# Kernel optimization log

Measured on AMD Instinct MI355X. Metric: run time of the kernel, lower is better.

## Reference

```python
import jax, jax.numpy as jnp
import numpy as np

B, L, D, H = 2, 2048, 512, 8
SAMPLING_FACTOR = 5


def setup_inputs() -> dict:
    key = jax.random.key(0)
    ks = jax.random.split(key, 12)
    L_K = min(8000, L)
    log_L_K = int(np.ceil(np.log1p(L_K)))
    U_part = min(SAMPLING_FACTOR * L * log_L_K, L_K)  # = 2048
    inp = {
        'q': jax.random.normal(ks[0], (B, L, D), jnp.float32),
        'k': jax.random.normal(ks[1], (B, L, D), jnp.float32),
        'v': jax.random.normal(ks[2], (B, L, D), jnp.float32),
        'Wq': jax.random.normal(ks[3], (D, D), jnp.float32) * 0.02,
        'bq': jnp.zeros((D,), jnp.float32),
        'Wk': jax.random.normal(ks[4], (D, D), jnp.float32) * 0.02,
        'bk': jnp.zeros((D,), jnp.float32),
        'Wv': jax.random.normal(ks[5], (D, D), jnp.float32) * 0.02,
        'bv': jnp.zeros((D,), jnp.float32),
        'Wo': jax.random.normal(ks[6], (D, D), jnp.float32) * 0.02,
        'bo': jnp.zeros((D,), jnp.float32),
        'index_sample': jax.random.randint(ks[7], (U_part,), 0, L_K, jnp.int32),
    }
    return inp


def _prob_sparse(qh, Kh, Vh, index_sample):
    # qh, Kh, Vh: [B, H, L, d]
    L_K = min(8000, Kh.shape[2])  # K_sample = K[:, :8000]; L_K = its length
    L_Q = qh.shape[2]
    Ks = Kh[:, :, index_sample, :]                                  # [B,H,U,d]
    QKs = jnp.einsum('bhqd,bhkd->bhqk', qh, Ks)                     # [B,H,Lq,U]
    # M = max - sum/L_K  (source divides by L_K, not U_part)
    M = QKs.max(axis=-1) - QKs.sum(axis=-1) / L_K                   # [B,H,Lq]
    u = min(SAMPLING_FACTOR * int(np.ceil(np.log1p(L_Q))), L_Q)     # = 40
    _, M_top = jax.lax.top_k(-M, u)                                 # topk(largest=False)
    Q_red = jnp.take_along_axis(qh, M_top[..., None], axis=2)       # [B,H,u,d]
    d_k = qh.shape[-1]
    scores = jnp.einsum('bhqd,bhkd->bhqk', Q_red, Kh) / jnp.sqrt(jnp.asarray(d_k, qh.dtype))
    probs = jax.nn.softmax(scores, axis=-1)
    out = jnp.einsum('bhqk,bhkd->bhqd', probs, Vh)                  # [B,H,u,d]
    return out, scores


def reference(q, k, v, Wq, bq, Wk, bk, Wv, bv, Wo, bo, index_sample):
    qp = q @ Wq.T + bq
    kp = k @ Wk.T + bk
    vp = v @ Wv.T + bv
    Bsz, Lq, Dm = qp.shape
    d = Dm // H
    # faithful to source: q is view'd to [B,H,Lq,d] WITHOUT transpose
    qh = qp.reshape(Bsz, H, Lq, d)
    kh = kp.reshape(Bsz, -1, H, d).transpose(0, 2, 1, 3)
    vh = vp.reshape(Bsz, -1, H, d).transpose(0, 2, 1, 3)
    out, _ = _prob_sparse(qh, kh, vh, index_sample)
    u = out.shape[2]
    out = out.transpose(0, 2, 1, 3).reshape(Bsz, u, Dm)             # concat
    return out @ Wo.T + bo                                          # [B,u,D]
```

## Files before the change

### kernel.cpp

```cpp
#include <hip/hip_runtime.h>
#include <math.h>

#define B_ 2
#define L_ 2048
#define D_ 512
#define H_ 8
#define DH 64
#define NS 2048
#define NU 40
#define BHD (L_*D_)
#define QHS (L_*DH)
#define WSPM 786432

typedef __attribute__((ext_vector_type(8))) short bf16x8;
typedef __attribute__((ext_vector_type(4))) float f32x4;

__device__ inline float4 ld4(const float* p) { return *reinterpret_cast<const float4*>(p); }

__device__ inline unsigned short hi16(float x) { return (unsigned short)(__float_as_uint(x) >> 16); }
__device__ inline float trunchf(float x) { return __uint_as_float(__float_as_uint(x) & 0xFFFF0000u); }
__device__ inline void tsplit(float x, unsigned short& hs, unsigned short& ms, unsigned short& ls) {
  float h = trunchf(x); hs = hi16(x);
  float r = x - h;
  float m = trunchf(r); ms = hi16(r);
  float r2 = r - m;
  ls = hi16(r2);
}

__global__ __launch_bounds__(256) void wsplit(const float* __restrict__ Wq,
                                              const float* __restrict__ Wk,
                                              const float* __restrict__ Wv,
                                              unsigned short* __restrict__ dst,
                                              int matArg) {
  const int mat = (matArg >= 0) ? matArg : (int)blockIdx.y;
  const float* W = (mat == 0) ? Wq : (mat == 1) ? Wk : Wv;
  unsigned short* d = dst + ((matArg >= 0) ? 0 : (size_t)mat * WSPM);
  const int t = threadIdx.x;
  const int nt = blockIdx.x >> 3, g16 = blockIdx.x & 7;
  const int kc = t >> 4, lr = t & 15;
  const int n = nt*128 + g16*16 + lr;
  const float* src = W + (size_t)n*512 + kc*32;
  float xs[32];
#pragma unroll
  for (int i = 0; i < 8; ++i) {
    float4 v4 = ld4(src + 4*i);
    xs[4*i] = v4.x; xs[4*i+1] = v4.y; xs[4*i+2] = v4.z; xs[4*i+3] = v4.w;
  }
  unsigned short Hs[32], Ms[32], Ls[32];
#pragma unroll
  for (int e = 0; e < 32; ++e) tsplit(xs[e], Hs[e], Ms[e], Ls[e]);
#pragma unroll
  for (int p = 0; p < 3; ++p) {
    const unsigned short* sp = (p == 0) ? Hs : (p == 1) ? Ms : Ls;
    unsigned short* base = d + ((size_t)((p*4 + nt)*8 + g16)*16 + kc)*512;
#pragma unroll
    for (int lg = 0; lg < 4; ++lg) {
      union { bf16x8 v; unsigned short u[8]; } P;
#pragma unroll
      for (int e = 0; e < 8; ++e) P.u[e] = sp[lg*8 + e];
      *reinterpret_cast<bf16x8*>(base + (lr + 16*lg)*8) = P.v;
    }
  }
}

__global__ __launch_bounds__(256) void proj_mfma2(
    const float* __restrict__ qa, const float* __restrict__ ka, const float* __restrict__ va,
    const unsigned short* __restrict__ wsp,
    const float* __restrict__ bq, const float* __restrict__ bk, const float* __restrict__ bv,
    float* __restrict__ qp, float* __restrict__ kp, float* __restrict__ vp,
    int matArg)
{
  __shared__ __align__(16) unsigned short a3[3][128][36];
  const int t = threadIdx.x;
  const int mat = (matArg >= 0) ? matArg : (int)blockIdx.z;
  const float* A    = (mat == 0) ? qa : (mat == 1) ? ka : va;
  const float* bias = (mat == 0) ? bq : (mat == 1) ? bk : bv;
  float* C          = (mat == 0) ? qp : (mat == 1) ? kp : vp;
  const unsigned short* wspm = wsp + ((matArg >= 0) ? 0 : (size_t)mat * WSPM);
  const int m0 = blockIdx.x * 128, nt = blockIdx.y;
  const int w = t >> 6, l = t & 63;
  const int wm = w >> 1, wn = w & 1;
  const int lr = l & 15, lg = l >> 4;
  const int srow = t >> 1, sc0 = (t & 1) * 16;

  f32x4 acc[4][4];
#pragma unroll
  for (int i = 0; i < 4; ++i)
#pragma unroll
    for (int j = 0; j < 4; ++j) acc[i][j] = (f32x4){0.f, 0.f, 0.f, 0.f};

  for (int kc = 0; kc < 16; ++kc) {
    __syncthreads();
    bf16x8 bw[3][4];
#pragma unroll
    for (int p = 0; p < 3; ++p)
#pragma unroll
      for (int ni = 0; ni < 4; ++ni)
        bw[p][ni] = *reinterpret_cast<const bf16x8*>(
            wspm + ((size_t)((p*4 + nt)*8 + wn*4 + ni)*16 + kc)*512 + l*8);
    {
      const float* src = A + (size_t)(m0 + srow) * 512 + kc*32 + sc0;
      float xs[16];
#pragma unroll
      for (int i = 0; i < 4; ++i) {
        float4 v4 = ld4(src + 4*i);
        xs[4*i] = v4.x; xs[4*i+1] = v4.y; xs[4*i+2] = v4.z; xs[4*i+3] = v4.w;
      }
#pragma unroll
      for (int hh = 0; hh < 2; ++hh) {
        union { bf16x8 v; unsigned short u[8]; } H, M, L;
#pragma unroll
        for (int e = 0; e < 8; ++e) tsplit(xs[hh*8 + e], H.u[e], M.u[e], L.u[e]);
        *reinterpret_cast<bf16x8*>(&a3[0][srow][sc0 + 8*hh]) = H.v;
        *reinterpret_cast<bf16x8*>(&a3[1][srow][sc0 + 8*hh]) = M.v;
        *reinterpret_cast<bf16x8*>(&a3[2][srow][sc0 + 8*hh]) = L.v;
      }
    }
    __syncthreads();

#pragma unroll
    for (int mi = 0; mi < 4; ++mi) {
      bf16x8 a0 = *reinterpret_cast<const bf16x8*>(&a3[0][wm*64 + mi*16 + lr][lg*8]);
      bf16x8 a1 = *reinterpret_cast<const bf16x8*>(&a3[1][wm*64 + mi*16 + lr][lg*8]);
      bf16x8 a2 = *reinterpret_cast<const bf16x8*>(&a3[2][wm*64 + mi*16 + lr][lg*8]);
#pragma unroll
      for (int ni = 0; ni < 4; ++ni) {
        acc[mi][ni] = __builtin_amdgcn_mfma_f32_16x16x32_bf16(a0, bw[0][ni], acc[mi][ni], 0, 0, 0);
        acc[mi][ni] = __builtin_amdgcn_mfma_f32_16x16x32_bf16(a0, bw[1][ni], acc[mi][ni], 0, 0, 0);
        acc[mi][ni] = __builtin_amdgcn_mfma_f32_16x16x32_bf16(a1, bw[0][ni], acc[mi][ni], 0, 0, 0);
        acc[mi][ni] = __builtin_amdgcn_mfma_f32_16x16x32_bf16(a1, bw[1][ni], acc[mi][ni], 0, 0, 0);
        acc[mi][ni] = __builtin_amdgcn_mfma_f32_16x16x32_bf16(a0, bw[2][ni], acc[mi][ni], 0, 0, 0);
        acc[mi][ni] = __builtin_amdgcn_mfma_f32_16x16x32_bf16(a2, bw[0][ni], acc[mi][ni], 0, 0, 0);
      }
    }
  }
#pragma unroll
  for (int mi = 0; mi < 4; ++mi)
#pragma unroll
    for (int ni = 0; ni < 4; ++ni) {
      const int gn = nt*128 + wn*64 + ni*16 + lr;
      const float bv_ = bias[gn];
#pragma unroll
      for (int r = 0; r < 4; ++r) {
        const int gm = m0 + wm*64 + mi*16 + lg*4 + r;
        C[(size_t)gm * 512 + gn] = acc[mi][ni][r] + bv_;
      }
    }
}

__global__ __launch_bounds__(1024) void ksum_kernel(const float* __restrict__ kp,
                                                    const int* __restrict__ idx,
                                                    float* __restrict__ ksum) {
  __shared__ float part[16][64];
  const int bh = blockIdx.x;
  const int b = bh >> 3, h = bh & 7;
  const int t = threadIdx.x;
  const int sg = t >> 6, j = t & 63;
  const float* kbase = kp + (size_t)b*BHD + h*DH;
  float a = 0.f;
  for (int s = sg*128; s < sg*128 + 128; ++s)
    a += kbase[(size_t)idx[s]*512 + j];
  part[sg][j] = a;
  __syncthreads();
  if (t < 64) {
    float s = 0.f;
#pragma unroll
    for (int i = 0; i < 16; ++i) s += part[i][t];
    ksum[bh*64 + t] = s;
  }
}

__global__ __launch_bounds__(256, 2) void m_kernel(const float* __restrict__ qp,
                                                   const float* __restrict__ kp,
                                                   const int* __restrict__ idx,
                                                   float* __restrict__ Mp) {
  __shared__ __align__(16) unsigned short k3[3][128][72];
  const int t = threadIdx.x;
  const int bid = blockIdx.x;
  const int bh = bid >> 5, qt = (bid >> 2) & 7, ks = bid & 3;
  const int b = bh >> 3, h = bh & 7;
  const int w = t >> 6, l = t & 63;
  const int lr = l & 15;
  const int lg = l >> 4;

  bf16x8 qf[4][2][3];
  {
    const float* qbase = qp + (size_t)b*BHD + (size_t)h*QHS + (size_t)(qt*256 + w*64 + lr) * 64 + lg*8;
#pragma unroll
    for (int mi = 0; mi < 4; ++mi)
#pragma unroll
      for (int c = 0; c < 2; ++c) {
        const float* src = qbase + mi*16*64 + c*32;
        float4 x0 = ld4(src), x1 = ld4(src + 4);
        float xs[8] = {x0.x, x0.y, x0.z, x0.w, x1.x, x1.y, x1.z, x1.w};
        union { bf16x8 v; unsigned short u[8]; } H, M, L;
#pragma unroll
        for (int e = 0; e < 8; ++e) tsplit(xs[e], H.u[e], M.u[e], L.u[e]);
        qf[mi][c][0] = H.v; qf[mi][c][1] = M.v; qf[mi][c][2] = L.v;
      }
  }

  const float* kbase = kp + (size_t)b*BHD + h*DH;
  const int ib = ks * 512;
  const int srow = t >> 1, sh = (t & 1) * 32;

  float4 vst[8];
  {
    const int kr = idx[ib + srow];
    const float* src = kbase + (size_t)kr * 512 + sh;
#pragma unroll
    for (int i = 0; i < 8; ++i) vst[i] = ld4(src + 4*i);
  }

  float mx[4][4];
#pragma unroll
  for (int mi = 0; mi < 4; ++mi)
#pragma unroll
    for (int r = 0; r < 4; ++r) mx[mi][r] = -INFINITY;

  for (int tl = 0; tl < 4; ++tl) {
    __syncthreads();
    {
#pragma unroll
      for (int e2 = 0; e2 < 4; ++e2) {
        union { bf16x8 v; unsigned short u[8]; } H, M, L;
        float xs[8] = {vst[2*e2].x, vst[2*e2].y, vst[2*e2].z, vst[2*e2].w,
                       vst[2*e2+1].x, vst[2*e2+1].y, vst[2*e2+1].z, vst[2*e2+1].w};
#pragma unroll
        for (int e = 0; e < 8; ++e) tsplit(xs[e], H.u[e], M.u[e], L.u[e]);
        *reinterpret_cast<bf16x8*>(&k3[0][srow][sh + 8*e2]) = H.v;
        *reinterpret_cast<bf16x8*>(&k3[1][srow][sh + 8*e2]) = M.v;
        *reinterpret_cast<bf16x8*>(&k3[2][srow][sh + 8*e2]) = L.v;
      }
    }
    if (tl < 3) {
      const int kr = idx[ib + (tl+1)*128 + srow];
      const float* src = kbase + (size_t)kr * 512 + sh;
#pragma unroll
      for (int i = 0; i < 8; ++i) vst[i] = ld4(src + 4*i);
    }
    __syncthreads();

    for (int n2 = 0; n2 < 4; ++n2) {
      bf16x8 bf[2][3][2];
#pragma unroll
      for (int ns = 0; ns < 2; ++ns)
#pragma unroll
        for (int p = 0; p < 3; ++p)
#pragma unroll
          for (int c = 0; c < 2; ++c)
            bf[ns][p][c] = *reinterpret_cast<const bf16x8*>(&k3[p][n2*32 + ns*16 + lr][c*32 + lg*8]);
      __builtin_amdgcn_s_setprio(1);
#pragma unroll
      for (int mi = 0; mi < 4; ++mi)
#pragma unroll
        for (int ns = 0; ns < 2; ++ns) {
          f32x4 acc = {0.f, 0.f, 0.f, 0.f};
#pragma unroll
          for (int c = 0; c < 2; ++c) acc = __builtin_amdgcn_mfma_f32_16x16x32_bf16(qf[mi][c][0], bf[ns][0][c], acc, 0, 0, 0);
#pragma unroll
          for (int c = 0; c < 2; ++c) acc = __builtin_amdgcn_mfma_f32_16x16x32_bf16(qf[mi][c][0], bf[ns][1][c], acc, 0, 0, 0);
#pragma unroll
          for (int c = 0; c < 2; ++c) acc = __builtin_amdgcn_mfma_f32_16x16x32_bf16(qf[mi][c][1], bf[ns][0][c], acc, 0, 0, 0);
#pragma unroll
          for (int c = 0; c < 2; ++c) acc = __builtin_amdgcn_mfma_f32_16x16x32_bf16(qf[mi][c][1], bf[ns][1][c], acc, 0, 0, 0);
#pragma unroll
          for (int c = 0; c < 2; ++c) acc = __builtin_amdgcn_mfma_f32_16x16x32_bf16(qf[mi][c][0], bf[ns][2][c], acc, 0, 0, 0);
#pragma unroll
          for (int c = 0; c < 2; ++c) acc = __builtin_amdgcn_mfma_f32_16x16x32_bf16(qf[mi][c][2], bf[ns][0][c], acc, 0, 0, 0);
#pragma unroll
          for (int r = 0; r < 4; ++r) mx[mi][r] = fmaxf(mx[mi][r], acc[r]);
        }
      __builtin_amdgcn_s_setprio(0);
    }
  }

#pragma unroll
  for (int mi = 0; mi < 4; ++mi)
#pragma unroll
    for (int r = 0; r < 4; ++r) {
      float v = mx[mi][r];
      v = fmaxf(v, __shfl_xor(v, 1));
      v = fmaxf(v, __shfl_xor(v, 2));
      v = fmaxf(v, __shfl_xor(v, 4));
      v = fmaxf(v, __shfl_xor(v, 8));
      if (lr == 0)
        Mp[ks*32768 + bh*2048 + qt*256 + w*64 + mi*16 + lg*4 + r] = v;
    }
}

__global__ __launch_bounds__(256) void topk_kernel(const float* __restrict__ qp,
                                                   const float* __restrict__ ksum,
                                                   const float* __restrict__ Mp,
                                                   int* __restrict__ Mtop) {
  __shared__ float ks_s[64];
  __shared__ unsigned hist[256];
  __shared__ int wsum[4];
  __shared__ unsigned bitmap[64];
  __shared__ unsigned long long comb[NU];
  __shared__ int s_sel, s_rem, s_cnt;
  const int bh = blockIdx.x;
  const int b = bh >> 3, h = bh & 7;
  const int t = threadIdx.x;
  if (t < 64) ks_s[t] = ksum[bh*64 + t];
  __syncthreads();

  unsigned mykey[8];
#pragma unroll
  for (int c = 0; c < 8; ++c) {
    const int qi = c * 256 + t;
    const float* qrow = qp + (size_t)b*BHD + (size_t)h*QHS + (size_t)qi * 64;
    float dot = 0.f;
#pragma unroll
    for (int cc = 0; cc < 16; ++cc) {
      float4 q4 = ld4(qrow + 4 * cc);
      dot += q4.x * ks_s[4*cc + 0];
      dot += q4.y * ks_s[4*cc + 1];
      dot += q4.z * ks_s[4*cc + 2];
      dot += q4.w * ks_s[4*cc + 3];
    }
    const float mx2 = fmaxf(fmaxf(Mp[bh*2048 + qi], Mp[32768 + bh*2048 + qi]),
                            fmaxf(Mp[65536 + bh*2048 + qi], Mp[98304 + bh*2048 + qi]));
    const float m = mx2 - dot * (1.0f/2048.0f);
    const unsigned u = __float_as_uint(m);
    mykey[c] = (u >> 31) ? ~u : (u | 0x80000000u);
  }

  unsigned prefMask = 0u, prefVal = 0u;
  int rem = NU;
  for (int shift = 24; shift >= 0; shift -= 8) {
    hist[t] = 0;
    __syncthreads();
#pragma unroll
    for (int c = 0; c < 8; ++c) {
      const unsigned key = mykey[c];
      if ((key & prefMask) == prefVal)
        atomicAdd(&hist[(key >> shift) & 255], 1u);
    }
    __syncthreads();
    const int binc = (int)hist[t];
    int inc = binc;
#pragma unroll
    for (int off = 1; off < 64; off <<= 1) {
      const int nb = __shfl_up(inc, off);
      if ((t & 63) >= off) inc += nb;
    }
    if ((t & 63) == 63) wsum[t >> 6] = inc;
    __syncthreads();
    int wadd = 0;
    for (int w2 = 0; w2 < (t >> 6); ++w2) wadd += wsum[w2];
    const int incl = inc + wadd;
    const int excl = incl - binc;
    if (excl < rem && rem <= incl) { s_sel = t; s_rem = rem - excl; }
    __syncthreads();
    prefVal |= ((unsigned)s_sel) << shift;
    prefMask |= 0xFFu << shift;
    rem = s_rem;
    __syncthreads();
  }
  const unsigned T = prefVal;

  if (t < 64) bitmap[t] = 0;
  if (t == 0) s_cnt = 0;
  __syncthreads();
#pragma unroll
  for (int c = 0; c < 8; ++c) {
    const unsigned key = mykey[c];
    const int qi = c * 256 + t;
    if (key < T) {
      const int pos = atomicAdd(&s_cnt, 1);
      comb[pos] = ((unsigned long long)key << 11) | (unsigned)qi;
    } else if (key == T) {
      atomicOr(&bitmap[qi >> 5], 1u << (qi & 31));
    }
  }
  __syncthreads();
  if (t == 0) {
    int need = rem, cpos = s_cnt;
    for (int wd = 0; wd < 64 && need > 0; ++wd) {
      unsigned bits = bitmap[wd];
      while (bits && need > 0) {
        const int bit = __ffs(bits) - 1;
        bits &= bits - 1;
        comb[cpos++] = ((unsigned long long)T << 11) | (unsigned)(wd*32 + bit);
        --need;
      }
    }
  }
  __syncthreads();

  if (t < 64) {
    const unsigned long long mine = (t < NU) ? comb[t] : ~0ULL;
    int rank = 0;
#pragma unroll
    for (int step = 1; step < 64; ++step) {
      const unsigned long long other = __shfl(mine, (t + step) & 63);
      rank += (other < mine) ? 1 : 0;
    }
    if (t < NU) Mtop[bh*NU + rank] = (int)(mine & 0x7FFu);
  }
}

__global__ __launch_bounds__(256) void flash_partial(const float* __restrict__ qp,
                                                     const float* __restrict__ kp,
                                                     const float* __restrict__ vp,
                                                     const int* __restrict__ Mtop,
                                                     float* __restrict__ pm,
                                                     float* __restrict__ pl,
                                                     float* __restrict__ pacc) {
  __shared__ float qr[NU][65];
  __shared__ float kv[64][65];
  __shared__ float sl[NU][65];
  __shared__ float ms[NU], ls[NU], fs[NU];
  const int bid = blockIdx.x;
  const int bh = bid >> 4, kt = bid & 15;
  const int b = bh >> 3, h = bh & 7;
  const int t = threadIdx.x;
  const int g = t >> 6, j = t & 63;
  const int r4 = t >> 2, sub = t & 3;

  {
    const float* qbase = qp + (size_t)b*BHD + (size_t)h*QHS;
#pragma unroll
    for (int r = 0; r < 10; ++r) {
      const int q = g*10 + r;
      qr[q][j] = qbase[(size_t)Mtop[bh*NU + q]*64 + j];
    }
  }
  if (t < NU) { ms[t] = -INFINITY; ls[t] = 0.f; }
  float acc[10];
#pragma unroll
  for (int r = 0; r < 10; ++r) acc[r] = 0.f;

  const float* kbase = kp + (size_t)b*BHD + h*DH;
  const float* vbase = vp + (size_t)b*BHD + h*DH;
  const int srow = t >> 2, scb = (t & 3)*16;

  for (int st = 0; st < 2; ++st) {
    const int kb = kt*128 + st*64;
    __syncthreads();
    {
      const float* src = kbase + (size_t)(kb + srow)*512 + scb;
#pragma unroll
      for (int i = 0; i < 4; ++i) {
        float4 v = ld4(src + 4*i);
        kv[srow][scb + 4*i + 0] = v.x;
        kv[srow][scb + 4*i + 1] = v.y;
        kv[srow][scb + 4*i + 2] = v.z;
        kv[srow][scb + 4*i + 3] = v.w;
      }
    }
    __syncthreads();
    {
      float sv[10];
#pragma unroll
      for (int r = 0; r < 10; ++r) {
        const int q = g*10 + r;
        float s = 0.f;
#pragma unroll 8
        for (int jj = 0; jj < 64; ++jj) s += qr[q][jj]*kv[j][jj];
        sv[r] = s * 0.125f;
      }
#pragma unroll
      for (int r = 0; r < 10; ++r) sl[g*10 + r][j] = sv[r];
    }
    __syncthreads();
    float4 vst[4];
    {
      const float* src = vbase + (size_t)(kb + srow)*512 + scb;
#pragma unroll
      for (int i = 0; i < 4; ++i) vst[i] = ld4(src + 4*i);
    }
    if (r4 < NU) {
      float tm = -INFINITY;
#pragma unroll
      for (int c = 0; c < 16; ++c) tm = fmaxf(tm, sl[r4][sub*16 + c]);
      tm = fmaxf(tm, __shfl_xor(tm, 1));
      tm = fmaxf(tm, __shfl_xor(tm, 2));
      const float nm = fmaxf(ms[r4], tm);
      if (sub == 0) { fs[r4] = expf(ms[r4] - nm); ms[r4] = nm; }
    }
    __syncthreads();
    {
#pragma unroll
      for (int r = 0; r < 10; ++r) {
        const int q = g*10 + r;
        acc[r] *= fs[q];
        sl[q][j] = expf(sl[q][j] - ms[q]);
      }
#pragma unroll
      for (int i = 0; i < 4; ++i) {
        kv[srow][scb + 4*i + 0] = vst[i].x;
        kv[srow][scb + 4*i + 1] = vst[i].y;
        kv[srow][scb + 4*i + 2] = vst[i].z;
        kv[srow][scb + 4*i + 3] = vst[i].w;
      }
    }
    __syncthreads();
    if (r4 < NU) {
      float s = 0.f;
#pragma unroll
      for (int c = 0; c < 16; ++c) s += sl[r4][sub*16 + c];
      s += __shfl_xor(s, 1);
      s += __shfl_xor(s, 2);
      if (sub == 0) ls[r4] = ls[r4]*fs[r4] + s;
    }
    {
#pragma unroll 4
      for (int kk = 0; kk < 64; ++kk) {
        const float vv = kv[kk][j];
#pragma unroll
        for (int r = 0; r < 10; ++r) acc[r] += sl[g*10 + r][kk]*vv;
      }
    }
  }
  __syncthreads();
  const size_t base = (size_t)(bh*16 + kt)*NU;
  if (t < NU) { pm[base + t] = ms[t]; pl[base + t] = ls[t]; }
#pragma unroll
  for (int r = 0; r < 10; ++r)
    pacc[(base + g*10 + r)*64 + j] = acc[r];
}

__global__ __launch_bounds__(256) void flash_combine(const float* __restrict__ pm,
                                                     const float* __restrict__ pl,
                                                     const float* __restrict__ pacc,
                                                     float* __restrict__ outc) {
  const int t = threadIdx.x;
  const int qg = t >> 6, j = t & 63;
  const int bh = blockIdx.x / 10;
  const int q  = (blockIdx.x % 10)*4 + qg;
  const int b = bh >> 3, h = bh & 7;
  float m = -INFINITY;
#pragma unroll
  for (int kt = 0; kt < 16; ++kt) m = fmaxf(m, pm[(size_t)(bh*16 + kt)*NU + q]);
  float Lsum = 0.f, num = 0.f;
#pragma unroll
  for (int kt = 0; kt < 16; ++kt) {
    const size_t base = (size_t)(bh*16 + kt)*NU;
    const float w = expf(pm[base + q] - m);
    Lsum += w * pl[base + q];
    num  += w * pacc[(base + q)*64 + j];
  }
  outc[(size_t)(b*NU + q)*512 + h*64 + j] = num / Lsum;
}

__global__ __launch_bounds__(256) void wo_gemm(const float* __restrict__ outc,
                                               const float* __restrict__ Wo,
                                               float* __restrict__ pwo) {
  __shared__ __align__(16) float a_t[80][68];
  __shared__ __align__(16) float w_t[64][68];
  const int t = threadIdx.x;
  const int ty = t >> 4, tx = t & 15;
  const int nt = blockIdx.x, ks = blockIdx.y;
  float acc[5][4];
#pragma unroll
  for (int i = 0; i < 5; ++i)
#pragma unroll
    for (int j = 0; j < 4; ++j) acc[i][j] = 0.f;

  for (int c = 0; c < 2; ++c) {
    const int kb = ks*128 + c*64;
    __syncthreads();
#pragma unroll
    for (int i = 0; i < 20; ++i) {
      const int fi = t + 256*i;
      const int row = fi >> 6, col = fi & 63;
      a_t[row][col] = outc[(size_t)row*512 + kb + col];
    }
#pragma unroll
    for (int i = 0; i < 16; ++i) {
      const int fi = t + 256*i;
      const int row = fi >> 6, col = fi & 63;
      w_t[row][col] = Wo[(size_t)(nt*64 + row)*512 + kb + col];
    }
    __syncthreads();
    for (int gq = 0; gq < 16; ++gq) {
      float4 av[5], wv[4];
#pragma unroll
      for (int i = 0; i < 5; ++i) av[i] = *reinterpret_cast<const float4*>(&a_t[ty + 16*i][4*gq]);
#pragma unroll
      for (int j = 0; j < 4; ++j) wv[j] = *reinterpret_cast<const float4*>(&w_t[tx + 16*j][4*gq]);
#pragma unroll
      for (int i = 0; i < 5; ++i)
#pragma unroll
        for (int j = 0; j < 4; ++j) {
          acc[i][j] += av[i].x * wv[j].x;
          acc[i][j] += av[i].y * wv[j].y;
          acc[i][j] += av[i].z * wv[j].z;
          acc[i][j] += av[i].w * wv[j].w;
        }
    }
  }
#pragma unroll
  for (int i = 0; i < 5; ++i)
#pragma unroll
    for (int j = 0; j < 4; ++j)
      pwo[ks*40960 + (size_t)(ty + 16*i)*512 + nt*64 + tx + 16*j] = acc[i][j];
}

__global__ __launch_bounds__(256) void wo_combine(const float* __restrict__ pwo,
                                                  const float* __restrict__ bo,
                                                  float* __restrict__ out) {
  const int gi = blockIdx.x*256 + threadIdx.x;
  const float4* p = reinterpret_cast<const float4*>(pwo);
  const float4 a = p[gi], b4 = p[10240 + gi], c4 = p[20480 + gi], d4 = p[30720 + gi];
  const float4 bb = ld4(bo + 4*(gi & 127));
  float4 o;
  o.x = a.x + b4.x + c4.x + d4.x + bb.x;
  o.y = a.y + b4.y + c4.y + d4.y + bb.y;
  o.z = a.z + b4.z + c4.z + d4.z + bb.z;
  o.w = a.w + b4.w + c4.w + d4.w + bb.w;
  reinterpret_cast<float4*>(out)[gi] = o;
}

extern "C" void kernel_launch(void* const* d_in, const int* in_sizes, int n_in,
                              void* d_out, int out_size, void* d_ws, size_t ws_size,
                              hipStream_t stream) {
  const float* q  = (const float*)d_in[0];
  const float* k  = (const float*)d_in[1];
  const float* v  = (const float*)d_in[2];
  const float* Wq = (const float*)d_in[3];
  const float* bq = (const float*)d_in[4];
  const float* Wk = (const float*)d_in[5];
  const float* bk = (const float*)d_in[6];
  const float* Wv = (const float*)d_in[7];
  const float* bv = (const float*)d_in[8];
  const float* Wo = (const float*)d_in[9];
  const float* bo = (const float*)d_in[10];
  const int*  idx = (const int*)d_in[11];

  float* ws   = (float*)d_ws;
  float* qp   = ws;
  float* kp   = ws + 2097152;
  float* vp   = ws + 4194304;
  float* ksum = ws + 6291456;
  int*   Mtop = (int*)(ws + 6292480);
  float* pm   = ws + 6293120;
  float* pl   = ws + 6303360;
  float* pacc = ws + 6313600;
  float* outc = ws + 6968960;
  float* Mp   = pm;
  float* pwo  = pm;
  unsigned short* wsp = (unsigned short*)(ws + 6291456);

  const dim3 blk(256);
  const bool bigws = (ws_size >= (size_t)7471104 * 4);
  if (bigws) {
    wsplit<<<dim3(32, 3), blk, 0, stream>>>(Wq, Wk, Wv, wsp, -1);
    proj_mfma2<<<dim3(32, 4, 3), blk, 0, stream>>>(q, k, v, wsp, bq, bk, bv, qp, kp, vp, -1);
  } else {
    for (int m = 0; m < 3; ++m) {
      wsplit<<<dim3(32, 1), blk, 0, stream>>>(Wq, Wk, Wv, wsp, m);
      proj_mfma2<<<dim3(32, 4, 1), blk, 0, stream>>>(q, k, v, wsp, bq, bk, bv, qp, kp, vp, m);
    }
  }
  ksum_kernel<<<dim3(16), dim3(1024), 0, stream>>>(kp, idx, ksum);
  m_kernel<<<dim3(512), blk, 0, stream>>>(qp, kp, idx, Mp);
  topk_kernel<<<dim3(16), blk, 0, stream>>>(qp, ksum, Mp, Mtop);
  flash_partial<<<dim3(256), blk, 0, stream>>>(qp, kp, vp, Mtop, pm, pl, pacc);
  flash_combine<<<dim3(160), blk, 0, stream>>>(pm, pl, pacc, outc);
  wo_gemm<<<dim3(8, 4), blk, 0, stream>>>(outc, Wo, pwo);
  wo_combine<<<dim3(40), blk, 0, stream>>>(pwo, bo, (float*)d_out);
}
```

Before: 190.2 us.

## Convert projection and M kernels to single-wave blocks loading operands directly

The projection GEMM and the M-score kernel are rewritten so each block is one 64-thread wave. Each wave loads its own fp32 A/K fragments from global memory and splits them into three bf16 parts in registers. This drops the shared-memory staging and the __syncthreads barriers. The cost is redundant global loads and repeated split arithmetic: A rows are re-read by 8 waves across N and sampled K rows by 32 query waves, with no software prefetch, so performance leans on cache hits and latency hiding through occupancy.

Measured after the change: 208.1 us. 9.4% more time.

```diff
diff --git a/kernel.cpp b/kernel.cpp
--- a/kernel.cpp
+++ b/kernel.cpp
@@ -25,6 +25,12 @@
   float m = trunchf(r); ms = hi16(r);
   float r2 = r - m;
   ls = hi16(r2);
+}
+__device__ inline void split8(const float* xs, bf16x8& a0, bf16x8& a1, bf16x8& a2) {
+  union { bf16x8 v; unsigned short u[8]; } H, M, L;
+#pragma unroll
+  for (int e = 0; e < 8; ++e) tsplit(xs[e], H.u[e], M.u[e], L.u[e]);
+  a0 = H.v; a1 = M.v; a2 = L.v;
 }
 
 __global__ __launch_bounds__(256) void wsplit(const float* __restrict__ Wq,
@@ -63,25 +69,24 @@
   }
 }
 
-__global__ __launch_bounds__(256) void proj_mfma2(
+__global__ __launch_bounds__(64, 3) void proj_wave(
     const float* __restrict__ qa, const float* __restrict__ ka, const float* __restrict__ va,
     const unsigned short* __restrict__ wsp,
     const float* __restrict__ bq, const float* __restrict__ bk, const float* __restrict__ bv,
-    float* __restrict__ qp, float* __restrict__ kp, float* __restrict__ vp,
-    int matArg)
+    float* __restrict__ qp, float* __restrict__ kp, float* __restrict__ vp, int matArg)
 {
-  __shared__ __align__(16) unsigned short a3[3][128][36];
-  const int t = threadIdx.x;
-  const int mat = (matArg >= 0) ? matArg : (int)blockIdx.z;
+  const int wid = blockIdx.x;
+  const int mat = (matArg >= 0) ? matArg : (wid >> 9);
+  const int rem = wid & 511;
+  const int wm = rem >> 3;
+  const int wn = rem & 7;
   const float* A    = (mat == 0) ? qa : (mat == 1) ? ka : va;
   const float* bias = (mat == 0) ? bq : (mat == 1) ? bk : bv;
   float* C          = (mat == 0) ? qp : (mat == 1) ? kp : vp;
   const unsigned short* wspm = wsp + ((matArg >= 0) ? 0 : (size_t)mat * WSPM);
-  const int m0 = blockIdx.x * 128, nt = blockIdx.y;
-  const int w = t >> 6, l = t & 63;
-  const int wm = w >> 1, wn = w & 1;
+  const int l = threadIdx.x;
   const int lr = l & 15, lg = l >> 4;
-  const int srow = t >> 1, sc0 = (t & 1) * 16;
+  const int m0 = wm * 64;
 
   f32x4 acc[4][4];
 #pragma unroll
@@ -90,39 +95,21 @@
     for (int j = 0; j < 4; ++j) acc[i][j] = (f32x4){0.f, 0.f, 0.f, 0.f};
 
   for (int kc = 0; kc < 16; ++kc) {
-    __syncthreads();
     bf16x8 bw[3][4];
 #pragma unroll
     for (int p = 0; p < 3; ++p)
 #pragma unroll
       for (int ni = 0; ni < 4; ++ni)
         bw[p][ni] = *reinterpret_cast<const bf16x8*>(
-            wspm + ((size_t)((p*4 + nt)*8 + wn*4 + ni)*16 + kc)*512 + l*8);
-    {
-      const float* src = A + (size_t)(m0 + srow) * 512 + kc*32 + sc0;
-      float xs[16];
-#pragma unroll
-      for (int i = 0; i < 4; ++i) {
-        float4 v4 = ld4(src + 4*i);
-        xs[4*i] = v4.x; xs[4*i+1] = v4.y; xs[4*i+2] = v4.z; xs[4*i+3] = v4.w;
-      }
-#pragma unroll
-      for (int hh = 0; hh < 2; ++hh) {
-        union { bf16x8 v; unsigned short u[8]; } H, M, L;
-#pragma unroll
-        for (int e = 0; e < 8; ++e) tsplit(xs[hh*8 + e], H.u[e], M.u[e], L.u[e]);
-        *reinterpret_cast<bf16x8*>(&a3[0][srow][sc0 + 8*hh]) = H.v;
-        *reinterpret_cast<bf16x8*>(&a3[1][srow][sc0 + 8*hh]) = M.v;
-        *reinterpret_cast<bf16x8*>(&a3[2][srow][sc0 + 8*hh]) = L.v;
-      }
-    }
-    __syncthreads();
-
+            wspm + ((size_t)((p*4 + (wn >> 1))*8 + (wn & 1)*4 + ni)*16 + kc)*512 + l*8);
 #pragma unroll
     for (int mi = 0; mi < 4; ++mi) {
-      bf16x8 a0 = *reinterpret_cast<const bf16x8*>(&a3[0][wm*64 + mi*16 + lr][lg*8]);
-      bf16x8 a1 = *reinterpret_cast<const bf16x8*>(&a3[1][wm*64 + mi*16 + lr][lg*8]);
-      bf16x8 a2 = *reinterpret_cast<const bf16x8*>(&a3[2][wm*64 + mi*16 + lr][lg*8]);
+      const float* src = A + (size_t)(m0 + mi*16 + lr)*512 + kc*32 + lg*8;
+      float4 x0 = ld4(src), x1 = ld4(src + 4);
+      float xs[8] = {x0.x, x0.y, x0.z, x0.w, x1.x, x1.y, x1.z, x1.w};
+      bf16x8 a0, a1, a2;
+      split8(xs, a0, a1, a2);
+      __builtin_amdgcn_s_setprio(1);
 #pragma unroll
       for (int ni = 0; ni < 4; ++ni) {
         acc[mi][ni] = __builtin_amdgcn_mfma_f32_16x16x32_bf16(a0, bw[0][ni], acc[mi][ni], 0, 0, 0);
@@ -132,17 +119,18 @@
         acc[mi][ni] = __builtin_amdgcn_mfma_f32_16x16x32_bf16(a0, bw[2][ni], acc[mi][ni], 0, 0, 0);
         acc[mi][ni] = __builtin_amdgcn_mfma_f32_16x16x32_bf16(a2, bw[0][ni], acc[mi][ni], 0, 0, 0);
       }
+      __builtin_amdgcn_s_setprio(0);
     }
   }
 #pragma unroll
   for (int mi = 0; mi < 4; ++mi)
 #pragma unroll
     for (int ni = 0; ni < 4; ++ni) {
-      const int gn = nt*128 + wn*64 + ni*16 + lr;
+      const int gn = wn*64 + ni*16 + lr;
       const float bv_ = bias[gn];
 #pragma unroll
       for (int r = 0; r < 4; ++r) {
-        const int gm = m0 + wm*64 + mi*16 + lg*4 + r;
+        const int gm = m0 + mi*16 + lg*4 + r;
         C[(size_t)gm * 512 + gn] = acc[mi][ni][r] + bv_;
       }
     }
@@ -170,22 +158,20 @@
   }
 }
 
-__global__ __launch_bounds__(256, 2) void m_kernel(const float* __restrict__ qp,
-                                                   const float* __restrict__ kp,
-                                                   const int* __restrict__ idx,
-                                                   float* __restrict__ Mp) {
-  __shared__ __align__(16) unsigned short k3[3][128][72];
-  const int t = threadIdx.x;
-  const int bid = blockIdx.x;
-  const int bh = bid >> 5, qt = (bid >> 2) & 7, ks = bid & 3;
+__global__ __launch_bounds__(64, 2) void m_wave(const float* __restrict__ qp,
+                                                const float* __restrict__ kp,
+                                                const int* __restrict__ idx,
+                                                float* __restrict__ Mp) {
+  const int wid = blockIdx.x;
+  const int bh = wid >> 7, rem = wid & 127;
+  const int qt = rem >> 2, ks = rem & 3;
   const int b = bh >> 3, h = bh & 7;
-  const int w = t >> 6, l = t & 63;
-  const int lr = l & 15;
-  const int lg = l >> 4;
+  const int l = threadIdx.x;
+  const int lr = l & 15, lg = l >> 4;
 
   bf16x8 qf[4][2][3];
   {
-    const float* qbase = qp + (size_t)b*BHD + (size_t)h*QHS + (size_t)(qt*256 + w*64 + lr) * 64 + lg*8;
+    const float* qbase = qp + (size_t)b*BHD + (size_t)h*QHS + (size_t)(qt*64 + lr) * 64 + lg*8;
 #pragma unroll
     for (int mi = 0; mi < 4; ++mi)
 #pragma unroll
@@ -193,24 +179,12 @@
         const float* src = qbase + mi*16*64 + c*32;
         float4 x0 = ld4(src), x1 = ld4(src + 4);
         float xs[8] = {x0.x, x0.y, x0.z, x0.w, x1.x, x1.y, x1.z, x1.w};
-        union { bf16x8 v; unsigned short u[8]; } H, M, L;
-#pragma unroll
-        for (int e = 0; e < 8; ++e) tsplit(xs[e], H.u[e], M.u[e], L.u[e]);
-        qf[mi][c][0] = H.v; qf[mi][c][1] = M.v; qf[mi][c][2] = L.v;
+        split8(xs, qf[mi][c][0], qf[mi][c][1], qf[mi][c][2]);
       }
   }
 
   const float* kbase = kp + (size_t)b*BHD + h*DH;
   const int ib = ks * 512;
-  const int srow = t >> 1, sh = (t & 1) * 32;
-
-  float4 vst[8];
-  {
-    const int kr = idx[ib + srow];
-    const float* src = kbase + (size_t)kr * 512 + sh;
-#pragma unroll
-    for (int i = 0; i < 8; ++i) vst[i] = ld4(src + 4*i);
-  }
 
   float mx[4][4];
 #pragma unroll
@@ -218,61 +192,42 @@
 #pragma unroll
     for (int r = 0; r < 4; ++r) mx[mi][r] = -INFINITY;
 
-  for (int tl = 0; tl < 4; ++tl) {
-    __syncthreads();
-    {
-#pragma unroll
-      for (int e2 = 0; e2 < 4; ++e2) {
-        union { bf16x8 v; unsigned short u[8]; } H, M, L;
-        float xs[8] = {vst[2*e2].x, vst[2*e2].y, vst[2*e2].z, vst[2*e2].w,
-                       vst[2*e2+1].x, vst[2*e2+1].y, vst[2*e2+1].z, vst[2*e2+1].w};
-#pragma unroll
-        for (int e = 0; e < 8; ++e) tsplit(xs[e], H.u[e], M.u[e], L.u[e]);
-        *reinterpret_cast<bf16x8*>(&k3[0][srow][sh + 8*e2]) = H.v;
-        *reinterpret_cast<bf16x8*>(&k3[1][srow][sh + 8*e2]) = M.v;
-        *reinterpret_cast<bf16x8*>(&k3[2][srow][sh + 8*e2]) = L.v;
-      }
-    }
-    if (tl < 3) {
-      const int kr = idx[ib + (tl+1)*128 + srow];
-      const float* src = kbase + (size_t)kr * 512 + sh;
-#pragma unroll
-      for (int i = 0; i < 8; ++i) vst[i] = ld4(src + 4*i);
-    }
-    __syncthreads();
-
-    for (int n2 = 0; n2 < 4; ++n2) {
-      bf16x8 bf[2][3][2];
-#pragma unroll
-      for (int ns = 0; ns < 2; ++ns)
-#pragma unroll
-        for (int p = 0; p < 3; ++p)
-#pragma unroll
-          for (int c = 0; c < 2; ++c)
-            bf[ns][p][c] = *reinterpret_cast<const bf16x8*>(&k3[p][n2*32 + ns*16 + lr][c*32 + lg*8]);
-      __builtin_amdgcn_s_setprio(1);
-#pragma unroll
-      for (int mi = 0; mi < 4; ++mi)
-#pragma unroll
-        for (int ns = 0; ns < 2; ++ns) {
-          f32x4 acc = {0.f, 0.f, 0.f, 0.f};
-#pragma unroll
-          for (int c = 0; c < 2; ++c) acc = __builtin_amdgcn_mfma_f32_16x16x32_bf16(qf[mi][c][0], bf[ns][0][c], acc, 0, 0, 0);
-#pragma unroll
-          for (int c = 0; c < 2; ++c) acc = __builtin_amdgcn_mfma_f32_16x16x32_bf16(qf[mi][c][0], bf[ns][1][c], acc, 0, 0, 0);
-#pragma unroll
-          for (int c = 0; c < 2; ++c) acc = __builtin_amdgcn_mfma_f32_16x16x32_bf16(qf[mi][c][1], bf[ns][0][c], acc, 0, 0, 0);
-#pragma unroll
-          for (int c = 0; c < 2; ++c) acc = __builtin_amdgcn_mfma_f32_16x16x32_bf16(qf[mi][c][1], bf[ns][1][c], acc, 0, 0, 0);
-#pragma unroll
-          for (int c = 0; c < 2; ++c) acc = __builtin_amdgcn_mfma_f32_16x16x32_bf16(qf[mi][c][0], bf[ns][2][c], acc, 0, 0, 0);
-#pragma unroll
-          for (int c = 0; c < 2; ++c) acc = __builtin_amdgcn_mfma_f32_16x16x32_bf16(qf[mi][c][2], bf[ns][0][c], acc, 0, 0, 0);
-#pragma unroll
-          for (int r = 0; r < 4; ++r) mx[mi][r] = fmaxf(mx[mi][r], acc[r]);
-        }
-      __builtin_amdgcn_s_setprio(0);
-    }
+  for (int g = 0; g < 16; ++g) {
+    bf16x8 bf[2][3][2];
+#pragma unroll
+    for (int ns = 0; ns < 2; ++ns) {
+      const int kr = idx[ib + g*32 + ns*16 + lr];
+      const float* krow = kbase + (size_t)kr * 512;
+#pragma unroll
+      for (int c = 0; c < 2; ++c) {
+        const float* src = krow + c*32 + lg*8;
+        float4 x0 = ld4(src), x1 = ld4(src + 4);
+        float xs[8] = {x0.x, x0.y, x0.z, x0.w, x1.x, x1.y, x1.z, x1.w};
+        split8(xs, bf[ns][0][c], bf[ns][1][c], bf[ns][2][c]);
+      }
+    }
+    __builtin_amdgcn_s_setprio(1);
+#pragma unroll
+    for (int mi = 0; mi < 4; ++mi)
+#pragma unroll
+      for (int ns = 0; ns < 2; ++ns) {
+        f32x4 acc = {0.f, 0.f, 0.f, 0.f};
+#pragma unroll
+        for (int c = 0; c < 2; ++c) acc = __builtin_amdgcn_mfma_f32_16x16x32_bf16(qf[mi][c][0], bf[ns][0][c], acc, 0, 0, 0);
+#pragma unroll
+        for (int c = 0; c < 2; ++c) acc = __builtin_amdgcn_mfma_f32_16x16x32_bf16(qf[mi][c][0], bf[ns][1][c], acc, 0, 0, 0);
+#pragma unroll
+        for (int c = 0; c < 2; ++c) acc = __builtin_amdgcn_mfma_f32_16x16x32_bf16(qf[mi][c][1], bf[ns][0][c], acc, 0, 0, 0);
+#pragma unroll
+        for (int c = 0; c < 2; ++c) acc = __builtin_amdgcn_mfma_f32_16x16x32_bf16(qf[mi][c][1], bf[ns][1][c], acc, 0, 0, 0);
+#pragma unroll
+        for (int c = 0; c < 2; ++c) acc = __builtin_amdgcn_mfma_f32_16x16x32_bf16(qf[mi][c][0], bf[ns][2][c], acc, 0, 0, 0);
+#pragma unroll
+        for (int c = 0; c < 2; ++c) acc = __builtin_amdgcn_mfma_f32_16x16x32_bf16(qf[mi][c][2], bf[ns][0][c], acc, 0, 0, 0);
+#pragma unroll
+        for (int r = 0; r < 4; ++r) mx[mi][r] = fmaxf(mx[mi][r], acc[r]);
+      }
+    __builtin_amdgcn_s_setprio(0);
   }
 
 #pragma unroll
@@ -285,7 +240,7 @@
       v = fmaxf(v, __shfl_xor(v, 4));
       v = fmaxf(v, __shfl_xor(v, 8));
       if (lr == 0)
-        Mp[ks*32768 + bh*2048 + qt*256 + w*64 + mi*16 + lg*4 + r] = v;
+        Mp[ks*32768 + bh*2048 + qt*64 + mi*16 + lg*4 + r] = v;
     }
 }
 
@@ -645,18 +600,19 @@
   unsigned short* wsp = (unsigned short*)(ws + 6291456);
 
   const dim3 blk(256);
+  const dim3 wblk(64);
   const bool bigws = (ws_size >= (size_t)7471104 * 4);
   if (bigws) {
     wsplit<<<dim3(32, 3), blk, 0, stream>>>(Wq, Wk, Wv, wsp, -1);
-    proj_mfma2<<<dim3(32, 4, 3), blk, 0, stream>>>(q, k, v, wsp, bq, bk, bv, qp, kp, vp, -1);
+    proj_wave<<<dim3(1536), wblk, 0, stream>>>(q, k, v, wsp, bq, bk, bv, qp, kp, vp, -1);
   } else {
     for (int m = 0; m < 3; ++m) {
       wsplit<<<dim3(32, 1), blk, 0, stream>>>(Wq, Wk, Wv, wsp, m);
-      proj_mfma2<<<dim3(32, 4, 1), blk, 0, stream>>>(q, k, v, wsp, bq, bk, bv, qp, kp, vp, m);
+      proj_wave<<<dim3(512), wblk, 0, stream>>>(q, k, v, wsp, bq, bk, bv, qp, kp, vp, m);
     }
   }
   ksum_kernel<<<dim3(16), dim3(1024), 0, stream>>>(kp, idx, ksum);
-  m_kernel<<<dim3(512), blk, 0, stream>>>(qp, kp, idx, Mp);
+  m_wave<<<dim3(2048), wblk, 0, stream>>>(qp, kp, idx, Mp);
   topk_kernel<<<dim3(16), blk, 0, stream>>>(qp, ksum, Mp, Mtop);
   flash_partial<<<dim3(256), blk, 0, stream>>>(qp, kp, vp, Mtop, pm, pl, pacc);
   flash_combine<<<dim3(160), blk, 0, stream>>>(pm, pl, pacc, outc);
```

## Double-buffer projection GEMM LDS tiles and prefetch next activation chunk

Applied to the files above, without the earlier changes.

The projection kernel now double-buffers its shared-memory A tiles, cutting two barriers per k-step to one. It prefetches the next 32-column chunk of activations into registers while the MFMA loop runs on the current buffer, and raises wave priority around the MFMA section. It also adds an occupancy hint of 2 blocks per CU in launch_bounds. The goal is to hide global-load latency behind matrix math, at the cost of doubled LDS use and extra register pressure.

After: 189.8 us. About the same (-0.2%).

```diff
diff --git a/kernel.cpp b/kernel.cpp
--- a/kernel.cpp
+++ b/kernel.cpp
@@ -63,14 +63,14 @@
   }
 }
 
-__global__ __launch_bounds__(256) void proj_mfma2(
+__global__ __launch_bounds__(256, 2) void proj_pipe(
     const float* __restrict__ qa, const float* __restrict__ ka, const float* __restrict__ va,
     const unsigned short* __restrict__ wsp,
     const float* __restrict__ bq, const float* __restrict__ bk, const float* __restrict__ bv,
     float* __restrict__ qp, float* __restrict__ kp, float* __restrict__ vp,
     int matArg)
 {
-  __shared__ __align__(16) unsigned short a3[3][128][36];
+  __shared__ __align__(16) unsigned short a3[2][3][128][36];
   const int t = threadIdx.x;
   const int mat = (matArg >= 0) ? matArg : (int)blockIdx.z;
   const float* A    = (mat == 0) ? qa : (mat == 1) ? ka : va;
@@ -89,8 +89,24 @@
 #pragma unroll
     for (int j = 0; j < 4; ++j) acc[i][j] = (f32x4){0.f, 0.f, 0.f, 0.f};
 
+  const float* aRow = A + (size_t)(m0 + srow) * 512 + sc0;
+  float4 ar0 = ld4(aRow), ar1 = ld4(aRow + 4), ar2 = ld4(aRow + 8), ar3 = ld4(aRow + 12);
+
   for (int kc = 0; kc < 16; ++kc) {
-    __syncthreads();
+    const int cur = kc & 1;
+    {
+      float xs[16] = {ar0.x, ar0.y, ar0.z, ar0.w, ar1.x, ar1.y, ar1.z, ar1.w,
+                      ar2.x, ar2.y, ar2.z, ar2.w, ar3.x, ar3.y, ar3.z, ar3.w};
+#pragma unroll
+      for (int hh = 0; hh < 2; ++hh) {
+        union { bf16x8 v; unsigned short u[8]; } H, M, L;
+#pragma unroll
+        for (int e = 0; e < 8; ++e) tsplit(xs[hh*8 + e], H.u[e], M.u[e], L.u[e]);
+        *reinterpret_cast<bf16x8*>(&a3[cur][0][srow][sc0 + 8*hh]) = H.v;
+        *reinterpret_cast<bf16x8*>(&a3[cur][1][srow][sc0 + 8*hh]) = M.v;
+        *reinterpret_cast<bf16x8*>(&a3[cur][2][srow][sc0 + 8*hh]) = L.v;
+      }
+    }
     bf16x8 bw[3][4];
 #pragma unroll
     for (int p = 0; p < 3; ++p)
@@ -98,31 +114,17 @@
       for (int ni = 0; ni < 4; ++ni)
         bw[p][ni] = *reinterpret_cast<const bf16x8*>(
             wspm + ((size_t)((p*4 + nt)*8 + wn*4 + ni)*16 + kc)*512 + l*8);
-    {
-      const float* src = A + (size_t)(m0 + srow) * 512 + kc*32 + sc0;
-      float xs[16];
-#pragma unroll
-      for (int i = 0; i < 4; ++i) {
-        float4 v4 = ld4(src + 4*i);
-        xs[4*i] = v4.x; xs[4*i+1] = v4.y; xs[4*i+2] = v4.z; xs[4*i+3] = v4.w;
-      }
-#pragma unroll
-      for (int hh = 0; hh < 2; ++hh) {
-        union { bf16x8 v; unsigned short u[8]; } H, M, L;
-#pragma unroll
-        for (int e = 0; e < 8; ++e) tsplit(xs[hh*8 + e], H.u[e], M.u[e], L.u[e]);
-        *reinterpret_cast<bf16x8*>(&a3[0][srow][sc0 + 8*hh]) = H.v;
-        *reinterpret_cast<bf16x8*>(&a3[1][srow][sc0 + 8*hh]) = M.v;
-        *reinterpret_cast<bf16x8*>(&a3[2][srow][sc0 + 8*hh]) = L.v;
-      }
-    }
-    __syncthreads();
-
+    __syncthreads();
+    if (kc < 15) {
+      const float* src = A + (size_t)(m0 + srow) * 512 + (kc+1)*32 + sc0;
+      ar0 = ld4(src); ar1 = ld4(src + 4); ar2 = ld4(src + 8); ar3 = ld4(src + 12);
+    }
+    __builtin_amdgcn_s_setprio(1);
 #pragma unroll
     for (int mi = 0; mi < 4; ++mi) {
-      bf16x8 a0 = *reinterpret_cast<const bf16x8*>(&a3[0][wm*64 + mi*16 + lr][lg*8]);
-      bf16x8 a1 = *reinterpret_cast<const bf16x8*>(&a3[1][wm*64 + mi*16 + lr][lg*8]);
-      bf16x8 a2 = *reinterpret_cast<const bf16x8*>(&a3[2][wm*64 + mi*16 + lr][lg*8]);
+      bf16x8 a0 = *reinterpret_cast<const bf16x8*>(&a3[cur][0][wm*64 + mi*16 + lr][lg*8]);
+      bf16x8 a1 = *reinterpret_cast<const bf16x8*>(&a3[cur][1][wm*64 + mi*16 + lr][lg*8]);
+      bf16x8 a2 = *reinterpret_cast<const bf16x8*>(&a3[cur][2][wm*64 + mi*16 + lr][lg*8]);
 #pragma unroll
       for (int ni = 0; ni < 4; ++ni) {
         acc[mi][ni] = __builtin_amdgcn_mfma_f32_16x16x32_bf16(a0, bw[0][ni], acc[mi][ni], 0, 0, 0);
@@ -133,6 +135,7 @@
         acc[mi][ni] = __builtin_amdgcn_mfma_f32_16x16x32_bf16(a2, bw[0][ni], acc[mi][ni], 0, 0, 0);
       }
     }
+    __builtin_amdgcn_s_setprio(0);
   }
 #pragma unroll
   for (int mi = 0; mi < 4; ++mi)
@@ -648,11 +651,11 @@
   const bool bigws = (ws_size >= (size_t)7471104 * 4);
   if (bigws) {
     wsplit<<<dim3(32, 3), blk, 0, stream>>>(Wq, Wk, Wv, wsp, -1);
-    proj_mfma2<<<dim3(32, 4, 3), blk, 0, stream>>>(q, k, v, wsp, bq, bk, bv, qp, kp, vp, -1);
+    proj_pipe<<<dim3(32, 4, 3), blk, 0, stream>>>(q, k, v, wsp, bq, bk, bv, qp, kp, vp, -1);
   } else {
     for (int m = 0; m < 3; ++m) {
       wsplit<<<dim3(32, 1), blk, 0, stream>>>(Wq, Wk, Wv, wsp, m);
-      proj_mfma2<<<dim3(32, 4, 1), blk, 0, stream>>>(q, k, v, wsp, bq, bk, bv, qp, kp, vp, m);
+      proj_pipe<<<dim3(32, 4, 1), blk, 0, stream>>>(q, k, v, wsp, bq, bk, bv, qp, kp, vp, m);
     }
   }
   ksum_kernel<<<dim3(16), dim3(1024), 0, stream>>>(kp, idx, ksum);
```
